# Optimization experiments

Hardware: AMD Instinct MI355X
Metric: run time of the kernel (lower is better)

Reference implementation:

```python
import jax, jax.numpy as jnp
import numpy as np

BATCH, IN, OUT = 4096, 4096, 4096

def setup_inputs() -> dict:
    key = jax.random.key(0)
    kx, kw, kb = jax.random.split(key, 3)
    x = jax.random.normal(kx, (BATCH, IN), dtype=jnp.float32)
    weights = jax.random.normal(kw, (OUT, IN), dtype=jnp.float32)
    beta = jax.random.normal(kb, (1,), dtype=jnp.float32)
    return {"x": x, "weights": weights, "beta": beta}

def reference(x, weights, beta):
    # original: sum over input dim of broadcast multiply == x @ W^T
    row_sum = jnp.einsum('bi,oi->bo', x, weights)  # [batch, output]
    return jax.nn.relu(1.0 - beta + row_sum)
```

## Files before the change

kernel.cpp:

```cpp
#include <hip/hip_runtime.h>
#include <hip/hip_bf16.h>
#include <cstdint>
#include <cstddef>

#define MDIM 4096
#define NDIM 4096
#define KDIM 4096

#define BM 256
#define BN 256
#define BK 64
#define NT (KDIM / BK)

typedef __bf16 bf16_t;
typedef bf16_t bf16x8 __attribute__((ext_vector_type(8)));
typedef float f32x4 __attribute__((ext_vector_type(4)));

#define GLDS16(gsrc, ldst)                                                   \
    __builtin_amdgcn_global_load_lds(                                        \
        (__attribute__((address_space(1))) void*)(gsrc),                     \
        (__attribute__((address_space(3))) void*)(ldst), 16, 0, 0)

#define BAR()   __builtin_amdgcn_s_barrier()
#define LGKM0() asm volatile("s_waitcnt lgkmcnt(0)" ::: "memory")
#define VM4()   asm volatile("s_waitcnt vmcnt(4)" ::: "memory")
#define VM0()   asm volatile("s_waitcnt vmcnt(0)" ::: "memory")

__device__ __forceinline__ int swz(int q) { return q ^ (((q >> 7) & 7) << 4); }

__global__ void cvt_f32_to_bf16(const float* __restrict__ src,
                                bf16_t* __restrict__ dst, int n) {
    int idx = (blockIdx.x * blockDim.x + threadIdx.x) * 8;
    int stride = gridDim.x * blockDim.x * 8;
    for (int i = idx; i < n; i += stride) {
        const float4* s = reinterpret_cast<const float4*>(src + i);
        float4 a = s[0];
        float4 b = s[1];
        bf16x8 o;
        o[0] = (bf16_t)a.x; o[1] = (bf16_t)a.y;
        o[2] = (bf16_t)a.z; o[3] = (bf16_t)a.w;
        o[4] = (bf16_t)b.x; o[5] = (bf16_t)b.y;
        o[6] = (bf16_t)b.z; o[7] = (bf16_t)b.w;
        *reinterpret_cast<bf16x8*>(dst + i) = o;
    }
}


#define LOAD_A_HALF(MH, BUF) do {                                            \
  _Pragma("unroll") for (int mi = 0; mi < 4; ++mi)                           \
  _Pragma("unroll") for (int ko = 0; ko < 2; ++ko)                           \
    av[mi][ko] = *(const bf16x8*)(ldsb + ((BUF) << 16) + a_off[(MH)*4 + mi][ko]); \
} while (0)

#define LOAD_B_PAIR(NH, BUF) do {                                            \
  _Pragma("unroll") for (int ni = 0; ni < 2; ++ni)                           \
  _Pragma("unroll") for (int ko = 0; ko < 2; ++ko)                           \
    bv[(NH)*2 + ni][ko] = *(const bf16x8*)(ldsb + ((BUF) << 16) + b_off[(NH)*2 + ni][ko]); \
} while (0)

#define MFMA_QUAD(MH, NH) do {                                               \
  _Pragma("unroll") for (int mi = 0; mi < 4; ++mi)                           \
  _Pragma("unroll") for (int ni = 0; ni < 2; ++ni)                           \
  _Pragma("unroll") for (int ko = 0; ko < 2; ++ko)                           \
    acc[(MH)*4 + mi][(NH)*2 + ni] = __builtin_amdgcn_mfma_f32_16x16x32_bf16( \
        av[mi][ko], bv[(NH)*2 + ni][ko], acc[(MH)*4 + mi][(NH)*2 + ni], 0, 0, 0); \
} while (0)

__global__ __launch_bounds__(512, 2) void gemm256(const bf16_t* __restrict__ A,
                                                  const bf16_t* __restrict__ B,
                                                  const float* __restrict__ beta,
                                                  float* __restrict__ out) {
    extern __shared__ char ldsb[];

    const int tid    = threadIdx.x;
    const int wid    = tid >> 6;
    const int lane   = tid & 63;
    const int warp_m = wid >> 2;
    const int warp_n = wid & 3;
    const int lrow   = lane & 15;
    const int kgrp   = lane >> 4;

    const int bid  = blockIdx.x;
    const int sbid = (bid & 7) * 32 + (bid >> 3);
    const int brow = (sbid >> 4) * BM;
    const int bcol = (sbid & 15) * BN;

    const int p0 = tid * 16, p1 = (tid + 512) * 16;
    const int q0 = swz(p0), q1 = swz(p1);
    const int rh0 = q0 >> 7, ce0 = (q0 & 127) >> 1;
    const int rh1 = q1 >> 7, ce1 = (q1 & 127) >> 1;

    const bf16_t* gA = A + (size_t)brow * KDIM;
    const bf16_t* gB = B + (size_t)bcol * KDIM;

    auto stageA = [&](int t, int h) {
        const int slot = ((t & 1) << 16) | (h << 14);
        GLDS16(gA + (size_t)(h * 128 + rh0) * KDIM + t * BK + ce0, ldsb + slot + p0);
        GLDS16(gA + (size_t)(h * 128 + rh1) * KDIM + t * BK + ce1, ldsb + slot + p1);
    };
    auto stageB = [&](int t, int h) {
        const int slot = ((t & 1) << 16) | ((2 + h) << 14);
        GLDS16(gB + (size_t)(h * 128 + rh0) * KDIM + t * BK + ce0, ldsb + slot + p0);
        GLDS16(gB + (size_t)(h * 128 + rh1) * KDIM + t * BK + ce1, ldsb + slot + p1);
    };

    int a_off[8][2];
#pragma unroll
    for (int mi = 0; mi < 8; ++mi)
#pragma unroll
        for (int ko = 0; ko < 2; ++ko)
            a_off[mi][ko] = (warp_m << 14) +
                swz((mi * 16 + lrow) * 128 + (ko * 32 + kgrp * 8) * 2);
    int b_off[4][2];
#pragma unroll
    for (int ni = 0; ni < 4; ++ni)
#pragma unroll
        for (int ko = 0; ko < 2; ++ko)
            b_off[ni][ko] = ((2 + (warp_n >> 1)) << 14) +
                swz(((warp_n & 1) * 64 + ni * 16 + lrow) * 128 + (ko * 32 + kgrp * 8) * 2);

    f32x4 acc[8][4];
#pragma unroll
    for (int i = 0; i < 8; ++i)
#pragma unroll
        for (int j = 0; j < 4; ++j)
            acc[i][j] = (f32x4){0.f, 0.f, 0.f, 0.f};

    bf16x8 av[4][2];
    bf16x8 bv[4][2];

    stageA(0, 0); stageA(0, 1); stageB(0, 0); stageB(0, 1);
    stageA(1, 0); stageB(1, 0);
    VM4();
    BAR();

    for (int t = 0; t < NT; ++t) {
        const int buf = t & 1;
        LOAD_A_HALF(0, buf);
        LOAD_B_PAIR(0, buf);
        if (t + 1 < NT) stageA(t + 1, 1);
        BAR(); LGKM0();
        __builtin_amdgcn_s_setprio(1);
        MFMA_QUAD(0, 0);
        __builtin_amdgcn_s_setprio(0);
        BAR();
        LOAD_B_PAIR(1, buf);
        if (t + 1 < NT) stageB(t + 1, 1);
        BAR(); LGKM0();
        __builtin_amdgcn_s_setprio(1);
        MFMA_QUAD(0, 1);
        __builtin_amdgcn_s_setprio(0);
        BAR();
        LOAD_A_HALF(1, buf);
        if (t + 2 < NT) stageB(t + 2, 0);
        BAR(); LGKM0();
        __builtin_amdgcn_s_setprio(1);
        MFMA_QUAD(1, 0);
        __builtin_amdgcn_s_setprio(0);
        BAR();
        if (t + 2 < NT) stageA(t + 2, 0);
        BAR(); LGKM0();
        __builtin_amdgcn_s_setprio(1);
        MFMA_QUAD(1, 1);
        __builtin_amdgcn_s_setprio(0);
        if (t < NT - 2) { VM4(); } else { VM0(); }
        BAR();
    }

    const float bias = 1.0f - beta[0];
    float* outp = out + (size_t)(brow + warp_m * 128) * NDIM + bcol + warp_n * 64;
#pragma unroll
    for (int mi = 0; mi < 8; ++mi)
#pragma unroll
        for (int ni = 0; ni < 4; ++ni)
#pragma unroll
            for (int j = 0; j < 4; ++j) {
                const int r = mi * 16 + kgrp * 4 + j;
                const int c = ni * 16 + lrow;
                outp[(size_t)r * NDIM + c] = fmaxf(acc[mi][ni][j] + bias, 0.0f);
            }
}

__global__ void gemm_f32_fallback(const float* __restrict__ A,
                                  const float* __restrict__ B,
                                  const float* __restrict__ beta,
                                  float* __restrict__ out) {
    __shared__ float sA[16][17];
    __shared__ float sB[16][17];
    const int tx = threadIdx.x, ty = threadIdx.y;
    const int m = blockIdx.y * 16 + ty;
    const int n = blockIdx.x * 16 + tx;
    float acc = 0.f;
    for (int k0 = 0; k0 < KDIM; k0 += 16) {
        sA[ty][tx] = A[(size_t)m * KDIM + k0 + tx];
        sB[ty][tx] = B[(size_t)(blockIdx.x * 16 + ty) * KDIM + k0 + tx];
        __syncthreads();
#pragma unroll
        for (int k = 0; k < 16; ++k)
            acc += sA[ty][k] * sB[tx][k];
        __syncthreads();
    }
    float v = acc + 1.0f - beta[0];
    out[(size_t)m * NDIM + n] = fmaxf(v, 0.f);
}

extern "C" void kernel_launch(void* const* d_in, const int* in_sizes, int n_in,
                              void* d_out, int out_size, void* d_ws, size_t ws_size,
                              hipStream_t stream) {
    const float* x    = (const float*)d_in[0];
    const float* w    = (const float*)d_in[1];
    const float* beta = (const float*)d_in[2];
    float* out        = (float*)d_out;

    const size_t nelem = (size_t)MDIM * (size_t)KDIM;
    const size_t need  = 2 * nelem * sizeof(bf16_t);

    if (ws_size >= need) {
        bf16_t* xb = (bf16_t*)d_ws;
        bf16_t* wb = xb + nelem;
        hipFuncSetAttribute((const void*)gemm256,
                            hipFuncAttributeMaxDynamicSharedMemorySize, 131072);
        cvt_f32_to_bf16<<<2048, 256, 0, stream>>>(x, xb, (int)nelem);
        cvt_f32_to_bf16<<<2048, 256, 0, stream>>>(w, wb, (int)nelem);
        gemm256<<<256, 512, 131072, stream>>>(xb, wb, beta, out);
    } else {
        dim3 grid(NDIM / 16, MDIM / 16);
        gemm_f32_fallback<<<grid, dim3(16, 16), 0, stream>>>(x, w, beta, out);
    }
}
```

Baseline: 151.3 us.

## Halve barriers per K-tile and unroll main loop by two with fixed buffers

```diff
diff --git a/kernel.cpp b/kernel.cpp
--- a/kernel.cpp
+++ b/kernel.cpp
@@ -22,9 +22,10 @@
         (__attribute__((address_space(3))) void*)(ldst), 16, 0, 0)
 
 #define BAR()   __builtin_amdgcn_s_barrier()
-#define LGKM0() asm volatile("s_waitcnt lgkmcnt(0)" ::: "memory")
 #define VM4()   asm volatile("s_waitcnt vmcnt(4)" ::: "memory")
 #define VM0()   asm volatile("s_waitcnt vmcnt(0)" ::: "memory")
+#define PRIO1() __builtin_amdgcn_s_setprio(1)
+#define PRIO0() __builtin_amdgcn_s_setprio(0)
 
 __device__ __forceinline__ int swz(int q) { return q ^ (((q >> 7) & 7) << 4); }
 
@@ -66,6 +67,29 @@
         av[mi][ko], bv[(NH)*2 + ni][ko], acc[(MH)*4 + mi][(NH)*2 + ni], 0, 0, 0); \
 } while (0)
 
+#define TILE(T, BUF) do {                                                    \
+                                                                     \
+    BAR();                                                                   \
+    LOAD_A_HALF(0, BUF); LOAD_B_PAIR(0, BUF);                                \
+    if ((T) + 1 < NT) stA((T) + 1, (BUF) ^ 1, 1);                            \
+    PRIO1(); MFMA_QUAD(0, 0); PRIO0();                                       \
+                                                                     \
+    BAR();                                                                   \
+    LOAD_B_PAIR(1, BUF);                                                     \
+    if ((T) + 1 < NT) stB((T) + 1, (BUF) ^ 1, 1);                            \
+    PRIO1(); MFMA_QUAD(0, 1); PRIO0();                                       \
+                                                                     \
+    BAR();                                                                   \
+    LOAD_A_HALF(1, BUF);                                                     \
+    if ((T) + 2 < NT) stB((T) + 2, (BUF), 0);                                \
+    PRIO1(); MFMA_QUAD(1, 0); PRIO0();                                       \
+                                                                     \
+    BAR();                                                                   \
+    if ((T) + 2 < NT) stA((T) + 2, (BUF), 0);                                \
+    PRIO1(); MFMA_QUAD(1, 1); PRIO0();                                       \
+    if ((T) < NT - 2) { VM4(); } else { VM0(); }                             \
+} while (0)
+
 __global__ __launch_bounds__(512, 2) void gemm256(const bf16_t* __restrict__ A,
                                                   const bf16_t* __restrict__ B,
                                                   const float* __restrict__ beta,
@@ -93,15 +117,26 @@
     const bf16_t* gA = A + (size_t)brow * KDIM;
     const bf16_t* gB = B + (size_t)bcol * KDIM;
 
-    auto stageA = [&](int t, int h) {
-        const int slot = ((t & 1) << 16) | (h << 14);
-        GLDS16(gA + (size_t)(h * 128 + rh0) * KDIM + t * BK + ce0, ldsb + slot + p0);
-        GLDS16(gA + (size_t)(h * 128 + rh1) * KDIM + t * BK + ce1, ldsb + slot + p1);
+    int offA[2][2], offB[2][2];
+#pragma unroll
+    for (int h = 0; h < 2; ++h) {
+        offA[h][0] = (h * 128 + rh0) * KDIM + ce0;
+        offA[h][1] = (h * 128 + rh1) * KDIM + ce1;
+        offB[h][0] = offA[h][0];
+        offB[h][1] = offA[h][1];
+    }
+
+    auto stA = [&](int t, int buf, int h) {
+        const bf16_t* g = gA + t * BK;
+        char* d = ldsb + (buf << 16) + (h << 14);
+        GLDS16(g + offA[h][0], d + p0);
+        GLDS16(g + offA[h][1], d + p1);
     };
-    auto stageB = [&](int t, int h) {
-        const int slot = ((t & 1) << 16) | ((2 + h) << 14);
-        GLDS16(gB + (size_t)(h * 128 + rh0) * KDIM + t * BK + ce0, ldsb + slot + p0);
-        GLDS16(gB + (size_t)(h * 128 + rh1) * KDIM + t * BK + ce1, ldsb + slot + p1);
+    auto stB = [&](int t, int buf, int h) {
+        const bf16_t* g = gB + t * BK;
+        char* d = ldsb + (buf << 16) + ((2 + h) << 14);
+        GLDS16(g + offB[h][0], d + p0);
+        GLDS16(g + offB[h][1], d + p1);
     };
 
     int a_off[8][2];
@@ -129,42 +164,13 @@
     bf16x8 av[4][2];
     bf16x8 bv[4][2];
 
-    stageA(0, 0); stageA(0, 1); stageB(0, 0); stageB(0, 1);
-    stageA(1, 0); stageB(1, 0);
+    stA(0, 0, 0); stA(0, 0, 1); stB(0, 0, 0); stB(0, 0, 1);
+    stB(1, 1, 0); stA(1, 1, 0);
     VM4();
-    BAR();
-
-    for (int t = 0; t < NT; ++t) {
-        const int buf = t & 1;
-        LOAD_A_HALF(0, buf);
-        LOAD_B_PAIR(0, buf);
-        if (t + 1 < NT) stageA(t + 1, 1);
-        BAR(); LGKM0();
-        __builtin_amdgcn_s_setprio(1);
-        MFMA_QUAD(0, 0);
-        __builtin_amdgcn_s_setprio(0);
-        BAR();
-        LOAD_B_PAIR(1, buf);
-        if (t + 1 < NT) stageB(t + 1, 1);
-        BAR(); LGKM0();
-        __builtin_amdgcn_s_setprio(1);
-        MFMA_QUAD(0, 1);
-        __builtin_amdgcn_s_setprio(0);
-        BAR();
-        LOAD_A_HALF(1, buf);
-        if (t + 2 < NT) stageB(t + 2, 0);
-        BAR(); LGKM0();
-        __builtin_amdgcn_s_setprio(1);
-        MFMA_QUAD(1, 0);
-        __builtin_amdgcn_s_setprio(0);
-        BAR();
-        if (t + 2 < NT) stageA(t + 2, 0);
-        BAR(); LGKM0();
-        __builtin_amdgcn_s_setprio(1);
-        MFMA_QUAD(1, 1);
-        __builtin_amdgcn_s_setprio(0);
-        if (t < NT - 2) { VM4(); } else { VM0(); }
-        BAR();
+
+    for (int t = 0; t < NT; t += 2) {
+        TILE(t, 0);
+        TILE(t + 1, 1);
     }
 
     const float bias = 1.0f - beta[0];
```

Measured after the change: 175.3 us. 15.9% more time.
